# Performance work log

Measured on AMD Instinct MI355X. Metric: run time of the kernel, lower is better.

Reference implementation:

```python
import jax, jax.numpy as jnp
import numpy as np

D_MODEL = 512
NUM_HEADS = 8
D_K = D_MODEL // NUM_HEADS


def setup_inputs() -> dict:
    key = jax.random.key(0)
    kx, kq, kk, kv, ko = jax.random.split(key, 5)
    scale = 1.0 / np.sqrt(D_MODEL)
    return {
        "x": jax.random.normal(kx, (2, 4096, D_MODEL), dtype=jnp.float32),
        "Wq": jax.random.normal(kq, (D_MODEL, D_MODEL), dtype=jnp.float32) * scale,
        "Wk": jax.random.normal(kk, (D_MODEL, D_MODEL), dtype=jnp.float32) * scale,
        "Wv": jax.random.normal(kv, (D_MODEL, D_MODEL), dtype=jnp.float32) * scale,
        "Wo": jax.random.normal(ko, (D_MODEL, D_MODEL), dtype=jnp.float32) * scale,
    }


def reference(x, Wq, Wk, Wv, Wo):
    B, T, D = x.shape
    H, dk = NUM_HEADS, D_K
    # Linear(d,d, bias=False): y = x @ W.T ; weights stored [out,in] like torch
    q = (x @ Wq.T).reshape(B, T, H, dk).transpose(0, 2, 1, 3)  # [B,H,T,dk]
    k = (x @ Wk.T).reshape(B, T, H, dk).transpose(0, 2, 1, 3)
    v = (x @ Wv.T).reshape(B, T, H, dk).transpose(0, 2, 1, 3)
    scores = jnp.einsum("bhqd,bhkd->bhqk", q, k) / np.sqrt(dk)  # [B,H,T,T]
    probs = jax.nn.softmax(scores, axis=-1)
    o = jnp.einsum("bhqk,bhkd->bhqd", probs, v)  # [B,H,T,dk]
    o = o.transpose(0, 2, 1, 3).reshape(B, T, D)
    return o @ Wo.T
```

## Files before the change

### kernel.cpp

```cpp
#include <hip/hip_runtime.h>
#include <hip/hip_bf16.h>

#define SEQ 4096
#define DMODEL 512
#define HEADS 8
#define DK 64
#define BATCH 2
#define MTOT (BATCH * SEQ)
#define NBH (BATCH * HEADS)

typedef __attribute__((ext_vector_type(8))) short bh8;
typedef __attribute__((ext_vector_type(4))) float f4;
typedef __attribute__((ext_vector_type(16))) float f16x;
typedef __attribute__((ext_vector_type(2))) float f2;

#define MFMA(a, b, c)   __builtin_amdgcn_mfma_f32_16x16x32_bf16(a, b, c, 0, 0, 0)
#define MFMA32(a, b, c) __builtin_amdgcn_mfma_f32_32x32x16_bf16(a, b, c, 0, 0, 0)
#define GLL16(g, l) __builtin_amdgcn_global_load_lds( \
    (const __attribute__((address_space(1))) void*)(g), \
    (__attribute__((address_space(3))) void*)(l), 16, 0, 0)

__device__ __forceinline__ unsigned short f2b(float f) {
    union { float f; unsigned u; } v; v.f = f;
    unsigned r = v.u + 0x7fff + ((v.u >> 16) & 1);
    return (unsigned short)(r >> 16);
}

__device__ __forceinline__ unsigned cvtpk(float lo, float hi) {
    unsigned r;
    asm("v_cvt_pk_bf16_f32 %0, %1, %2" : "=v"(r) : "v"(lo), "v"(hi));
    return r;
}
__device__ __forceinline__ void plswap(unsigned& a, unsigned& b) {
    asm("v_permlane32_swap_b32 %0, %1" : "+v"(a), "+v"(b));
}
__device__ __forceinline__ float wave_max_pair(float x) {
    float b = x; asm("" : "+v"(b));
    float a = x;
    asm("v_permlane32_swap_b32 %0, %1" : "+v"(a), "+v"(b));
    return fmaxf(a, b);
}
__device__ __forceinline__ float wave_sum_pair(float x) {
    float b = x; asm("" : "+v"(b));
    float a = x;
    asm("v_permlane32_swap_b32 %0, %1" : "+v"(a), "+v"(b));
    return a + b;
}
__device__ __forceinline__ f2 pk_add(f2 a, f2 b) {
    f2 d; asm("v_pk_add_f32 %0, %1, %2" : "=v"(d) : "v"(a), "v"(b)); return d;
}
__device__ __forceinline__ f2 pk_mul(f2 a, f2 b) {
    f2 d; asm("v_pk_mul_f32 %0, %1, %2" : "=v"(d) : "v"(a), "v"(b)); return d;
}
__device__ __forceinline__ float max3f(float a, float b, float c) {
    float d; asm("v_max3_f32 %0, %1, %2, %3" : "=v"(d) : "v"(a), "v"(b), "v"(c));
    return d;
}

__global__ __launch_bounds__(256) void convert_k(
    const float* __restrict__ x, const float* __restrict__ wq,
    const float* __restrict__ wk, const float* __restrict__ wv,
    const float* __restrict__ wo, unsigned short* __restrict__ dst)
{
    const size_t i = ((size_t)blockIdx.x * 256 + threadIdx.x) * 4;
    const float* s; size_t o;
    if (i < 4194304u)                 { s = x;  o = i; }
    else if (i < 4194304u + 262144u)  { s = wq; o = i - 4194304u; }
    else if (i < 4194304u + 524288u)  { s = wk; o = i - (4194304u + 262144u); }
    else if (i < 4194304u + 786432u)  { s = wv; o = i - (4194304u + 524288u); }
    else                              { s = wo; o = i - (4194304u + 786432u); }
    float4 v = *(const float4*)(s + o);
    ushort4 u; u.x = f2b(v.x); u.y = f2b(v.y); u.z = f2b(v.z); u.w = f2b(v.w);
    *(ushort4*)(dst + i) = u;
}

__global__ __launch_bounds__(256) void qkv_gemm_mfma(
    const unsigned short* __restrict__ xb,
    const unsigned short* __restrict__ Wb,
    unsigned short* __restrict__ QKV)
{
    const int z = blockIdx.z;
    const unsigned short* A = xb;
    const unsigned short* B = Wb + (size_t)z * (DMODEL * DMODEL);
    const int m0 = blockIdx.x * 128, n0 = blockIdx.y * 128;
    const int tid = threadIdx.x, w = tid >> 6, l = tid & 63;
    const int wr = w >> 1, wc = w & 1;

    __shared__ __align__(16) unsigned short As[128 * 32];
    __shared__ __align__(16) unsigned short Bs[128 * 32];

    f4 acc[4][4] = {};
    const int lrow = l >> 2, lslot = l & 3;

    for (int k0 = 0; k0 < DMODEL; k0 += 32) {
        __syncthreads();
        #pragma unroll
        for (int j = 0; j < 2; ++j) {
            const int row = w * 32 + j * 16 + lrow;
            const int sw = lslot ^ ((row >> 1) & 3);
            GLL16(A + (size_t)(m0 + row) * DMODEL + k0 + sw * 8,
                  (char*)As + (w * 32 + j * 16) * 64);
            GLL16(B + (size_t)(n0 + row) * DMODEL + k0 + sw * 8,
                  (char*)Bs + (w * 32 + j * 16) * 64);
        }
        __syncthreads();
        bh8 af[4], bg[4];
        #pragma unroll
        for (int mi = 0; mi < 4; ++mi) {
            const int r = wr * 64 + mi * 16 + (l & 15);
            af[mi] = *(const bh8*)((const char*)As + r * 64 +
                                   (((l >> 4) * 16) ^ (((r >> 1) & 3) << 4)));
        }
        #pragma unroll
        for (int ni = 0; ni < 4; ++ni) {
            const int r = wc * 64 + ni * 16 + (l & 15);
            bg[ni] = *(const bh8*)((const char*)Bs + r * 64 +
                                   (((l >> 4) * 16) ^ (((r >> 1) & 3) << 4)));
        }
        #pragma unroll
        for (int mi = 0; mi < 4; ++mi)
            #pragma unroll
            for (int ni = 0; ni < 4; ++ni)
                acc[mi][ni] = MFMA(af[mi], bg[ni], acc[mi][ni]);
    }

    unsigned short* Out = QKV + (size_t)z * ((size_t)NBH * SEQ * DK);
    const float sc = (z == 0) ? 0.18033688011112042f : 1.0f;
    #pragma unroll
    for (int mi = 0; mi < 4; ++mi) {
        #pragma unroll
        for (int rg = 0; rg < 4; ++rg) {
            const int m = m0 + wr * 64 + mi * 16 + (l >> 4) * 4 + rg;
            const int b = m >> 12, t = m & (SEQ - 1);
            #pragma unroll
            for (int ni = 0; ni < 4; ++ni) {
                const int n = n0 + wc * 64 + ni * 16 + (l & 15);
                const int h = n >> 6, d = n & 63;
                Out[(((size_t)(b * HEADS + h)) * SEQ + t) * DK + d] =
                    f2b(acc[mi][ni][rg] * sc);
            }
        }
    }
}

__global__ __launch_bounds__(256) void vtrans(
    const unsigned short* __restrict__ Vh, unsigned short* __restrict__ Vt)
{
    const int bh = blockIdx.y, t0 = blockIdx.x * 64;
    __shared__ unsigned short L[64][72];
    const unsigned short* src = Vh + ((size_t)bh * SEQ + t0) * DK;
    const int r = threadIdx.x >> 3, c8 = (threadIdx.x & 7) * 8;
    #pragma unroll
    for (int it = 0; it < 2; ++it) {
        const int row = r + it * 32;
        ushort4 a = *(const ushort4*)(src + (size_t)row * DK + c8);
        ushort4 b = *(const ushort4*)(src + (size_t)row * DK + c8 + 4);
        L[row][c8 + 0] = a.x; L[row][c8 + 1] = a.y; L[row][c8 + 2] = a.z; L[row][c8 + 3] = a.w;
        L[row][c8 + 4] = b.x; L[row][c8 + 5] = b.y; L[row][c8 + 6] = b.z; L[row][c8 + 7] = b.w;
    }
    __syncthreads();
    unsigned short* dst = Vt + (size_t)bh * DK * SEQ + t0;
    #pragma unroll
    for (int it = 0; it < 2; ++it) {
        const int d = r + it * 32;
        ushort4 a, b;
        a.x = L[c8 + 0][d]; a.y = L[c8 + 1][d]; a.z = L[c8 + 2][d]; a.w = L[c8 + 3][d];
        b.x = L[c8 + 4][d]; b.y = L[c8 + 5][d]; b.z = L[c8 + 6][d]; b.w = L[c8 + 7][d];
        *(ushort4*)(dst + (size_t)d * SEQ + c8) = a;
        *(ushort4*)(dst + (size_t)d * SEQ + c8 + 4) = b;
    }
}

__global__ __launch_bounds__(256) void flash_mfma(
    const unsigned short* __restrict__ Qh,
    const unsigned short* __restrict__ Kh,
    const unsigned short* __restrict__ Vtp,
    unsigned short* __restrict__ Ow)
{
    const int bid = blockIdx.x;
    const int bh = bid & 15, q0 = (bid >> 4) * 128;
    const int tid = threadIdx.x, w = tid >> 6, l = tid & 63;
    const int lq = l & 31, hi = l >> 5;

    __shared__ __align__(16) char lds[32768];

    const unsigned short* Qb = Qh + (size_t)bh * SEQ * DK;
    const unsigned short* Kb = Kh + (size_t)bh * SEQ * DK;
    const unsigned short* Vb = Vtp + (size_t)bh * DK * SEQ;

    bh8 qf[4];
    #pragma unroll
    for (int ks = 0; ks < 4; ++ks)
        qf[ks] = *(const bh8*)(Qb + (size_t)(q0 + w * 32 + lq) * DK + ks * 16 + hi * 8);

    int koff[2], voff[2];
    #pragma unroll
    for (int j = 0; j < 2; ++j) {
        const int f = 2 * w + j, rh = f >> 2, ks = f & 3;
        koff[j] = (rh * 32 + lq) * DK + ks * 16 + hi * 8;
        voff[j] = (rh * 32 + lq) * SEQ + ks * 16 + hi * 8;
    }

    f16x o0 = {}, o1 = {};
    float m_run = -3.0e38f, l_run = 0.f;

#define STAGE(buf, kv0_) do {                                             \
    _Pragma("unroll")                                                     \
    for (int j_ = 0; j_ < 2; ++j_) {                                      \
        GLL16(Kb + (size_t)(kv0_) * DK + koff[j_],                        \
              lds + (buf) * 16384 + (2 * w + j_) * 1024);                 \
        GLL16(Vb + (size_t)(kv0_) + voff[j_],                             \
              lds + (buf) * 16384 + 8192 + (2 * w + j_) * 1024);          \
    }                                                                     \
} while (0)

    STAGE(0, 0);
    __syncthreads();
    int cur = 0;
    const char* myfrag = lds + l * 16;

    for (int t = 0; t < SEQ / 64; ++t) {
        if (t < SEQ / 64 - 1) STAGE(cur ^ 1, (t + 1) * 64);

        const char* kb = myfrag + cur * 16384;

        f16x sa0 = {}, sa1 = {};
        __builtin_amdgcn_s_setprio(1);
        #pragma unroll
        for (int ks = 0; ks < 4; ++ks) {
            bh8 k0 = *(const bh8*)(kb + ks * 1024);
            bh8 k1 = *(const bh8*)(kb + (4 + ks) * 1024);
            sa0 = MFMA32(k0, qf[ks], sa0);
            sa1 = MFMA32(k1, qf[ks], sa1);
        }
        __builtin_amdgcn_s_setprio(0);

        float a = fmaxf(sa0[0], sa0[1]);
        float b = fmaxf(sa1[0], sa1[1]);
        #pragma unroll
        for (int r = 2; r < 16; r += 2) {
            a = max3f(a, sa0[r], sa0[r + 1]);
            b = max3f(b, sa1[r], sa1[r + 1]);
        }
        const float mx = wave_max_pair(fmaxf(a, b));

        const bool skip = __all(mx <= m_run + 8.0f);
        float mnew = m_run, corr = 1.0f;
        if (!skip) {
            mnew = fmaxf(m_run, mx);
            corr = __builtin_amdgcn_exp2f(m_run - mnew);
        }

        union uf { f16x v; f2 h[8]; };
        uf U0, U1; U0.v = sa0; U1.v = sa1;
        f2 nm2; nm2[0] = -mnew; nm2[1] = -mnew;
        f2 p2[16];
        #pragma unroll
        for (int i = 0; i < 8; ++i) {
            f2 t0 = pk_add(U0.h[i], nm2);
            f2 t1 = pk_add(U1.h[i], nm2);
            f2 e0, e1;
            e0[0] = __builtin_amdgcn_exp2f(t0[0]);
            e0[1] = __builtin_amdgcn_exp2f(t0[1]);
            e1[0] = __builtin_amdgcn_exp2f(t1[0]);
            e1[1] = __builtin_amdgcn_exp2f(t1[1]);
            p2[i] = e0; p2[8 + i] = e1;
        }

        f2 s0 = pk_add(p2[0], p2[1]),   s1 = pk_add(p2[2], p2[3]);
        f2 s2 = pk_add(p2[4], p2[5]),   s3 = pk_add(p2[6], p2[7]);
        f2 s4 = pk_add(p2[8], p2[9]),   s5 = pk_add(p2[10], p2[11]);
        f2 s6 = pk_add(p2[12], p2[13]), s7 = pk_add(p2[14], p2[15]);
        s0 = pk_add(s0, s1); s2 = pk_add(s2, s3);
        s4 = pk_add(s4, s5); s6 = pk_add(s6, s7);
        s0 = pk_add(s0, s2); s4 = pk_add(s4, s6);
        s0 = pk_add(s0, s4);
        const float psum = wave_sum_pair(s0[0] + s0[1]);

        if (!skip) {
            m_run = mnew;
            l_run = l_run * corr + psum;
            f2 c2; c2[0] = corr; c2[1] = corr;
            uf O0, O1; O0.v = o0; O1.v = o1;
            #pragma unroll
            for (int i = 0; i < 8; ++i) {
                O0.h[i] = pk_mul(O0.h[i], c2);
                O1.h[i] = pk_mul(O1.h[i], c2);
            }
            o0 = O0.v; o1 = O1.v;
        } else {
            l_run += psum;
        }

        bh8 pf[4];
        #pragma unroll
        for (int cb = 0; cb < 2; ++cb) {
            unsigned k0 = cvtpk(p2[8 * cb + 0][0], p2[8 * cb + 0][1]);
            unsigned k1 = cvtpk(p2[8 * cb + 1][0], p2[8 * cb + 1][1]);
            unsigned k2 = cvtpk(p2[8 * cb + 2][0], p2[8 * cb + 2][1]);
            unsigned k3 = cvtpk(p2[8 * cb + 3][0], p2[8 * cb + 3][1]);
            unsigned k4 = cvtpk(p2[8 * cb + 4][0], p2[8 * cb + 4][1]);
            unsigned k5 = cvtpk(p2[8 * cb + 5][0], p2[8 * cb + 5][1]);
            unsigned k6 = cvtpk(p2[8 * cb + 6][0], p2[8 * cb + 6][1]);
            unsigned k7 = cvtpk(p2[8 * cb + 7][0], p2[8 * cb + 7][1]);
            plswap(k0, k2); plswap(k1, k3); plswap(k4, k6); plswap(k5, k7);
            union { unsigned u[4]; bh8 v; } f0, f1;
            f0.u[0] = k0; f0.u[1] = k1; f0.u[2] = k2; f0.u[3] = k3;
            f1.u[0] = k4; f1.u[1] = k5; f1.u[2] = k6; f1.u[3] = k7;
            pf[cb * 2 + 0] = f0.v;
            pf[cb * 2 + 1] = f1.v;
        }

        const char* vb = myfrag + cur * 16384 + 8192;
        __builtin_amdgcn_s_setprio(1);
        #pragma unroll
        for (int ks = 0; ks < 4; ++ks) {
            bh8 v0 = *(const bh8*)(vb + ks * 1024);
            bh8 v1 = *(const bh8*)(vb + (4 + ks) * 1024);
            o0 = MFMA32(v0, pf[ks], o0);
            o1 = MFMA32(v1, pf[ks], o1);
        }
        __builtin_amdgcn_s_setprio(0);

        __syncthreads();
        cur ^= 1;
    }
#undef STAGE

    const float inv = 1.0f / l_run;
    char* Tb = lds + w * 4096;
    #pragma unroll
    for (int db = 0; db < 2; ++db) {
        f16x ov = db ? o1 : o0;
        #pragma unroll
        for (int j = 0; j < 8; ++j) {
            const int r = 2 * j;
            const int d = db * 32 + (r & 3) + 8 * (r >> 2) + 4 * hi;
            unsigned pk = cvtpk(ov[r] * inv, ov[r + 1] * inv);
            *(unsigned*)(Tb + lq * 128 + ((d * 2) ^ ((lq & 7) << 4))) = pk;
        }
    }
    __syncthreads();
    const int b = bh >> 3, h = bh & 7;
    const int row = l >> 1, half = l & 1;
    const int q = q0 + w * 32 + row;
    unsigned short* dst = Ow + ((size_t)b * SEQ + q) * DMODEL + h * DK + half * 32;
    #pragma unroll
    for (int i = 0; i < 4; ++i) {
        const int byte = (half * 64 + i * 16) ^ ((row & 7) << 4);
        uint4 vv = *(const uint4*)(Tb + row * 128 + byte);
        *(uint4*)(dst + i * 8) = vv;
    }
}

__global__ __launch_bounds__(256) void out_gemm_mfma(
    const unsigned short* __restrict__ Ob,
    const unsigned short* __restrict__ Wob,
    float* __restrict__ out)
{
    const int m0 = blockIdx.x * 128, n0 = blockIdx.y * 128;
    const int tid = threadIdx.x, w = tid >> 6, l = tid & 63;
    const int wr = w >> 1, wc = w & 1;

    __shared__ __align__(16) unsigned short As[128 * 32];
    __shared__ __align__(16) unsigned short Bs[128 * 32];

    f4 acc[4][4] = {};
    const int lrow = l >> 2, lslot = l & 3;

    for (int k0 = 0; k0 < DMODEL; k0 += 32) {
        __syncthreads();
        #pragma unroll
        for (int j = 0; j < 2; ++j) {
            const int row = w * 32 + j * 16 + lrow;
            const int sw = lslot ^ ((row >> 1) & 3);
            GLL16(Ob + (size_t)(m0 + row) * DMODEL + k0 + sw * 8,
                  (char*)As + (w * 32 + j * 16) * 64);
            GLL16(Wob + (size_t)(n0 + row) * DMODEL + k0 + sw * 8,
                  (char*)Bs + (w * 32 + j * 16) * 64);
        }
        __syncthreads();
        bh8 af[4], bg[4];
        #pragma unroll
        for (int mi = 0; mi < 4; ++mi) {
            const int r = wr * 64 + mi * 16 + (l & 15);
            af[mi] = *(const bh8*)((const char*)As + r * 64 +
                                   (((l >> 4) * 16) ^ (((r >> 1) & 3) << 4)));
        }
        #pragma unroll
        for (int ni = 0; ni < 4; ++ni) {
            const int r = wc * 64 + ni * 16 + (l & 15);
            bg[ni] = *(const bh8*)((const char*)Bs + r * 64 +
                                   (((l >> 4) * 16) ^ (((r >> 1) & 3) << 4)));
        }
        #pragma unroll
        for (int mi = 0; mi < 4; ++mi)
            #pragma unroll
            for (int ni = 0; ni < 4; ++ni)
                acc[mi][ni] = MFMA(af[mi], bg[ni], acc[mi][ni]);
    }

    #pragma unroll
    for (int mi = 0; mi < 4; ++mi) {
        #pragma unroll
        for (int rg = 0; rg < 4; ++rg) {
            const int m = m0 + wr * 64 + mi * 16 + (l >> 4) * 4 + rg;
            #pragma unroll
            for (int ni = 0; ni < 4; ++ni) {
                const int n = n0 + wc * 64 + ni * 16 + (l & 15);
                out[(size_t)m * DMODEL + n] = acc[mi][ni][rg];
            }
        }
    }
}

extern "C" void kernel_launch(void* const* d_in, const int* in_sizes, int n_in,
                              void* d_out, int out_size, void* d_ws, size_t ws_size,
                              hipStream_t stream)
{
    const float* x  = (const float*)d_in[0];
    const float* Wq = (const float*)d_in[1];
    const float* Wk = (const float*)d_in[2];
    const float* Wv = (const float*)d_in[3];
    const float* Wo = (const float*)d_in[4];
    float* out = (float*)d_out;

    unsigned short* ws = (unsigned short*)d_ws;
    unsigned short* xb  = ws;
    unsigned short* Wb  = xb + 4194304;
    unsigned short* QKV = Wb + 4 * 262144;
    unsigned short* Vt  = QKV + 3 * 4194304;
    unsigned short* Ow  = Vt + 4194304;
    unsigned short* Qh = QKV;
    unsigned short* Kh = QKV + 4194304;
    unsigned short* Vh = QKV + 2 * 4194304;

    convert_k<<<5120, 256, 0, stream>>>(x, Wq, Wk, Wv, Wo, ws);
    qkv_gemm_mfma<<<dim3(MTOT / 128, DMODEL / 128, 3), 256, 0, stream>>>(xb, Wb, QKV);
    vtrans<<<dim3(SEQ / 64, NBH), 256, 0, stream>>>(Vh, Vt);
    flash_mfma<<<512, 256, 0, stream>>>(Qh, Kh, Vt, Ow);
    out_gemm_mfma<<<dim3(MTOT / 128, DMODEL / 128), 256, 0, stream>>>(
        Ow, Wb + 3 * 262144, out);
}
```

Baseline: 154.0 us.

## Split KV sequence into two interleaved streams with independent softmax states

Each wave now runs two independent online-softmax streams over the two halves of the key/value sequence, interleaving their QK^T and softmax/PV phases within every iteration, and merges them at the end with rescaling. This exposes more instruction-level parallelism so MFMA work of one stream can overlap with the exp/reduction work of the other, and halves the number of loop iterations and barriers. The cost is doubled LDS usage (64 KB) and more accumulator registers, which can lower occupancy. A launch-bounds hint of two blocks per CU is added.

```diff
diff --git a/kernel.cpp b/kernel.cpp
--- a/kernel.cpp
+++ b/kernel.cpp
@@ -13,6 +13,8 @@
 typedef __attribute__((ext_vector_type(4))) float f4;
 typedef __attribute__((ext_vector_type(16))) float f16x;
 typedef __attribute__((ext_vector_type(2))) float f2;
+
+union uf { f16x v; f2 h[8]; };
 
 #define MFMA(a, b, c)   __builtin_amdgcn_mfma_f32_16x16x32_bf16(a, b, c, 0, 0, 0)
 #define MFMA32(a, b, c) __builtin_amdgcn_mfma_f32_32x32x16_bf16(a, b, c, 0, 0, 0)
@@ -171,7 +173,7 @@
     }
 }
 
-__global__ __launch_bounds__(256) void flash_mfma(
+__global__ __launch_bounds__(256, 2) void flash_mfma(
     const unsigned short* __restrict__ Qh,
     const unsigned short* __restrict__ Kh,
     const unsigned short* __restrict__ Vtp,
@@ -182,7 +184,7 @@
     const int tid = threadIdx.x, w = tid >> 6, l = tid & 63;
     const int lq = l & 31, hi = l >> 5;
 
-    __shared__ __align__(16) char lds[32768];
+    __shared__ __align__(16) char lds[65536];
 
     const unsigned short* Qb = Qh + (size_t)bh * SEQ * DK;
     const unsigned short* Kb = Kh + (size_t)bh * SEQ * DK;
@@ -201,133 +203,151 @@
         voff[j] = (rh * 32 + lq) * SEQ + ks * 16 + hi * 8;
     }
 
-    f16x o0 = {}, o1 = {};
-    float m_run = -3.0e38f, l_run = 0.f;
-
-#define STAGE(buf, kv0_) do {                                             \
-    _Pragma("unroll")                                                     \
-    for (int j_ = 0; j_ < 2; ++j_) {                                      \
-        GLL16(Kb + (size_t)(kv0_) * DK + koff[j_],                        \
-              lds + (buf) * 16384 + (2 * w + j_) * 1024);                 \
-        GLL16(Vb + (size_t)(kv0_) + voff[j_],                             \
-              lds + (buf) * 16384 + 8192 + (2 * w + j_) * 1024);          \
-    }                                                                     \
+    f16x oA0 = {}, oA1 = {}, oB0 = {}, oB1 = {};
+    float mA = -3.0e38f, lA = 0.f, mB = -3.0e38f, lB = 0.f;
+
+#define STAGE(buf_, half_, kv0_) do {                                         \
+    _Pragma("unroll")                                                         \
+    for (int j_ = 0; j_ < 2; ++j_) {                                          \
+        GLL16(Kb + (size_t)(half_) * (2048 * DK) + (size_t)(kv0_) * DK + koff[j_], \
+              lds + (buf_) * 32768 + (half_) * 16384 + (2 * w + j_) * 1024);  \
+        GLL16(Vb + (half_) * 2048 + (size_t)(kv0_) + voff[j_],                \
+              lds + (buf_) * 32768 + (half_) * 16384 + 8192 + (2 * w + j_) * 1024); \
+    }                                                                         \
 } while (0)
 
-    STAGE(0, 0);
+#define QKT(kb_, sa0_, sa1_) do {                                             \
+    __builtin_amdgcn_s_setprio(1);                                            \
+    _Pragma("unroll")                                                         \
+    for (int ks_ = 0; ks_ < 4; ++ks_) {                                       \
+        bh8 k0_ = *(const bh8*)((kb_) + ks_ * 1024);                          \
+        bh8 k1_ = *(const bh8*)((kb_) + (4 + ks_) * 1024);                    \
+        sa0_ = MFMA32(k0_, qf[ks_], sa0_);                                    \
+        sa1_ = MFMA32(k1_, qf[ks_], sa1_);                                    \
+    }                                                                         \
+    __builtin_amdgcn_s_setprio(0);                                            \
+} while (0)
+
+#define SMPV(vb_, sa0_, sa1_, m_run_, l_run_, o0_, o1_) do {                  \
+    float a_ = fmaxf(sa0_[0], sa0_[1]);                                       \
+    float b_ = fmaxf(sa1_[0], sa1_[1]);                                       \
+    _Pragma("unroll")                                                         \
+    for (int r_ = 2; r_ < 16; r_ += 2) {                                      \
+        a_ = max3f(a_, sa0_[r_], sa0_[r_ + 1]);                               \
+        b_ = max3f(b_, sa1_[r_], sa1_[r_ + 1]);                               \
+    }                                                                         \
+    const float mx_ = wave_max_pair(fmaxf(a_, b_));                           \
+    const bool skip_ = __all(mx_ <= m_run_ + 8.0f);                           \
+    float mnew_ = m_run_, corr_ = 1.0f;                                       \
+    if (!skip_) {                                                             \
+        mnew_ = fmaxf(m_run_, mx_);                                           \
+        corr_ = __builtin_amdgcn_exp2f(m_run_ - mnew_);                       \
+    }                                                                         \
+    uf U0_, U1_; U0_.v = sa0_; U1_.v = sa1_;                                  \
+    f2 nm2_; nm2_[0] = -mnew_; nm2_[1] = -mnew_;                              \
+    f2 p2_[16];                                                               \
+    _Pragma("unroll")                                                         \
+    for (int i_ = 0; i_ < 8; ++i_) {                                          \
+        f2 t0_ = pk_add(U0_.h[i_], nm2_);                                     \
+        f2 t1_ = pk_add(U1_.h[i_], nm2_);                                     \
+        f2 e0_, e1_;                                                          \
+        e0_[0] = __builtin_amdgcn_exp2f(t0_[0]);                              \
+        e0_[1] = __builtin_amdgcn_exp2f(t0_[1]);                              \
+        e1_[0] = __builtin_amdgcn_exp2f(t1_[0]);                              \
+        e1_[1] = __builtin_amdgcn_exp2f(t1_[1]);                              \
+        p2_[i_] = e0_; p2_[8 + i_] = e1_;                                     \
+    }                                                                         \
+    f2 s0_ = pk_add(p2_[0], p2_[1]),   s1_ = pk_add(p2_[2], p2_[3]);          \
+    f2 s2_ = pk_add(p2_[4], p2_[5]),   s3_ = pk_add(p2_[6], p2_[7]);          \
+    f2 s4_ = pk_add(p2_[8], p2_[9]),   s5_ = pk_add(p2_[10], p2_[11]);        \
+    f2 s6_ = pk_add(p2_[12], p2_[13]), s7_ = pk_add(p2_[14], p2_[15]);        \
+    s0_ = pk_add(s0_, s1_); s2_ = pk_add(s2_, s3_);                           \
+    s4_ = pk_add(s4_, s5_); s6_ = pk_add(s6_, s7_);                           \
+    s0_ = pk_add(s0_, s2_); s4_ = pk_add(s4_, s6_);                           \
+    s0_ = pk_add(s0_, s4_);                                                   \
+    const float psum_ = wave_sum_pair(s0_[0] + s0_[1]);                       \
+    if (!skip_) {                                                             \
+        m_run_ = mnew_;                                                       \
+        l_run_ = l_run_ * corr_ + psum_;                                      \
+        f2 c2_; c2_[0] = corr_; c2_[1] = corr_;                               \
+        uf O0_, O1_; O0_.v = o0_; O1_.v = o1_;                                \
+        _Pragma("unroll")                                                     \
+        for (int i_ = 0; i_ < 8; ++i_) {                                      \
+            O0_.h[i_] = pk_mul(O0_.h[i_], c2_);                               \
+            O1_.h[i_] = pk_mul(O1_.h[i_], c2_);                               \
+        }                                                                     \
+        o0_ = O0_.v; o1_ = O1_.v;                                             \
+    } else {                                                                  \
+        l_run_ += psum_;                                                      \
+    }                                                                         \
+    bh8 pf_[4];                                                               \
+    _Pragma("unroll")                                                         \
+    for (int cb_ = 0; cb_ < 2; ++cb_) {                                       \
+        unsigned k0_ = cvtpk(p2_[8 * cb_ + 0][0], p2_[8 * cb_ + 0][1]);       \
+        unsigned k1_ = cvtpk(p2_[8 * cb_ + 1][0], p2_[8 * cb_ + 1][1]);       \
+        unsigned k2_ = cvtpk(p2_[8 * cb_ + 2][0], p2_[8 * cb_ + 2][1]);       \
+        unsigned k3_ = cvtpk(p2_[8 * cb_ + 3][0], p2_[8 * cb_ + 3][1]);       \
+        unsigned k4_ = cvtpk(p2_[8 * cb_ + 4][0], p2_[8 * cb_ + 4][1]);       \
+        unsigned k5_ = cvtpk(p2_[8 * cb_ + 5][0], p2_[8 * cb_ + 5][1]);       \
+        unsigned k6_ = cvtpk(p2_[8 * cb_ + 6][0], p2_[8 * cb_ + 6][1]);       \
+        unsigned k7_ = cvtpk(p2_[8 * cb_ + 7][0], p2_[8 * cb_ + 7][1]);       \
+        plswap(k0_, k2_); plswap(k1_, k3_); plswap(k4_, k6_); plswap(k5_, k7_);\
+        union { unsigned u[4]; bh8 v; } f0_, f1_;                             \
+        f0_.u[0] = k0_; f0_.u[1] = k1_; f0_.u[2] = k2_; f0_.u[3] = k3_;       \
+        f1_.u[0] = k4_; f1_.u[1] = k5_; f1_.u[2] = k6_; f1_.u[3] = k7_;       \
+        pf_[cb_ * 2 + 0] = f0_.v;                                             \
+        pf_[cb_ * 2 + 1] = f1_.v;                                             \
+    }                                                                         \
+    __builtin_amdgcn_s_setprio(1);                                            \
+    _Pragma("unroll")                                                         \
+    for (int ks_ = 0; ks_ < 4; ++ks_) {                                       \
+        bh8 v0_ = *(const bh8*)((vb_) + ks_ * 1024);                          \
+        bh8 v1_ = *(const bh8*)((vb_) + (4 + ks_) * 1024);                    \
+        o0_ = MFMA32(v0_, pf_[ks_], o0_);                                     \
+        o1_ = MFMA32(v1_, pf_[ks_], o1_);                                     \
+    }                                                                         \
+    __builtin_amdgcn_s_setprio(0);                                            \
+} while (0)
+
+    STAGE(0, 0, 0);
+    STAGE(0, 1, 0);
     __syncthreads();
     int cur = 0;
     const char* myfrag = lds + l * 16;
 
-    for (int t = 0; t < SEQ / 64; ++t) {
-        if (t < SEQ / 64 - 1) STAGE(cur ^ 1, (t + 1) * 64);
-
-        const char* kb = myfrag + cur * 16384;
-
-        f16x sa0 = {}, sa1 = {};
-        __builtin_amdgcn_s_setprio(1);
-        #pragma unroll
-        for (int ks = 0; ks < 4; ++ks) {
-            bh8 k0 = *(const bh8*)(kb + ks * 1024);
-            bh8 k1 = *(const bh8*)(kb + (4 + ks) * 1024);
-            sa0 = MFMA32(k0, qf[ks], sa0);
-            sa1 = MFMA32(k1, qf[ks], sa1);
-        }
-        __builtin_amdgcn_s_setprio(0);
-
-        float a = fmaxf(sa0[0], sa0[1]);
-        float b = fmaxf(sa1[0], sa1[1]);
-        #pragma unroll
-        for (int r = 2; r < 16; r += 2) {
-            a = max3f(a, sa0[r], sa0[r + 1]);
-            b = max3f(b, sa1[r], sa1[r + 1]);
-        }
-        const float mx = wave_max_pair(fmaxf(a, b));
-
-        const bool skip = __all(mx <= m_run + 8.0f);
-        float mnew = m_run, corr = 1.0f;
-        if (!skip) {
-            mnew = fmaxf(m_run, mx);
-            corr = __builtin_amdgcn_exp2f(m_run - mnew);
-        }
-
-        union uf { f16x v; f2 h[8]; };
-        uf U0, U1; U0.v = sa0; U1.v = sa1;
-        f2 nm2; nm2[0] = -mnew; nm2[1] = -mnew;
-        f2 p2[16];
-        #pragma unroll
-        for (int i = 0; i < 8; ++i) {
-            f2 t0 = pk_add(U0.h[i], nm2);
-            f2 t1 = pk_add(U1.h[i], nm2);
-            f2 e0, e1;
-            e0[0] = __builtin_amdgcn_exp2f(t0[0]);
-            e0[1] = __builtin_amdgcn_exp2f(t0[1]);
-            e1[0] = __builtin_amdgcn_exp2f(t1[0]);
-            e1[1] = __builtin_amdgcn_exp2f(t1[1]);
-            p2[i] = e0; p2[8 + i] = e1;
-        }
-
-        f2 s0 = pk_add(p2[0], p2[1]),   s1 = pk_add(p2[2], p2[3]);
-        f2 s2 = pk_add(p2[4], p2[5]),   s3 = pk_add(p2[6], p2[7]);
-        f2 s4 = pk_add(p2[8], p2[9]),   s5 = pk_add(p2[10], p2[11]);
-        f2 s6 = pk_add(p2[12], p2[13]), s7 = pk_add(p2[14], p2[15]);
-        s0 = pk_add(s0, s1); s2 = pk_add(s2, s3);
-        s4 = pk_add(s4, s5); s6 = pk_add(s6, s7);
-        s0 = pk_add(s0, s2); s4 = pk_add(s4, s6);
-        s0 = pk_add(s0, s4);
-        const float psum = wave_sum_pair(s0[0] + s0[1]);
-
-        if (!skip) {
-            m_run = mnew;
-            l_run = l_run * corr + psum;
-            f2 c2; c2[0] = corr; c2[1] = corr;
-            uf O0, O1; O0.v = o0; O1.v = o1;
-            #pragma unroll
-            for (int i = 0; i < 8; ++i) {
-                O0.h[i] = pk_mul(O0.h[i], c2);
-                O1.h[i] = pk_mul(O1.h[i], c2);
-            }
-            o0 = O0.v; o1 = O1.v;
-        } else {
-            l_run += psum;
-        }
-
-        bh8 pf[4];
-        #pragma unroll
-        for (int cb = 0; cb < 2; ++cb) {
-            unsigned k0 = cvtpk(p2[8 * cb + 0][0], p2[8 * cb + 0][1]);
-            unsigned k1 = cvtpk(p2[8 * cb + 1][0], p2[8 * cb + 1][1]);
-            unsigned k2 = cvtpk(p2[8 * cb + 2][0], p2[8 * cb + 2][1]);
-            unsigned k3 = cvtpk(p2[8 * cb + 3][0], p2[8 * cb + 3][1]);
-            unsigned k4 = cvtpk(p2[8 * cb + 4][0], p2[8 * cb + 4][1]);
-            unsigned k5 = cvtpk(p2[8 * cb + 5][0], p2[8 * cb + 5][1]);
-            unsigned k6 = cvtpk(p2[8 * cb + 6][0], p2[8 * cb + 6][1]);
-            unsigned k7 = cvtpk(p2[8 * cb + 7][0], p2[8 * cb + 7][1]);
-            plswap(k0, k2); plswap(k1, k3); plswap(k4, k6); plswap(k5, k7);
-            union { unsigned u[4]; bh8 v; } f0, f1;
-            f0.u[0] = k0; f0.u[1] = k1; f0.u[2] = k2; f0.u[3] = k3;
-            f1.u[0] = k4; f1.u[1] = k5; f1.u[2] = k6; f1.u[3] = k7;
-            pf[cb * 2 + 0] = f0.v;
-            pf[cb * 2 + 1] = f1.v;
-        }
-
-        const char* vb = myfrag + cur * 16384 + 8192;
-        __builtin_amdgcn_s_setprio(1);
-        #pragma unroll
-        for (int ks = 0; ks < 4; ++ks) {
-            bh8 v0 = *(const bh8*)(vb + ks * 1024);
-            bh8 v1 = *(const bh8*)(vb + (4 + ks) * 1024);
-            o0 = MFMA32(v0, pf[ks], o0);
-            o1 = MFMA32(v1, pf[ks], o1);
-        }
-        __builtin_amdgcn_s_setprio(0);
+    for (int t = 0; t < 32; ++t) {
+        if (t < 31) {
+            STAGE(cur ^ 1, 0, (t + 1) * 64);
+            STAGE(cur ^ 1, 1, (t + 1) * 64);
+        }
+
+        const char* kbA = myfrag + cur * 32768;
+        const char* kbB = kbA + 16384;
+
+        f16x sA0 = {}, sA1 = {}, sB0 = {}, sB1 = {};
+        QKT(kbA, sA0, sA1);
+        QKT(kbB, sB0, sB1);
+        SMPV(kbA + 8192, sA0, sA1, mA, lA, oA0, oA1);
+        SMPV(kbB + 8192, sB0, sB1, mB, lB, oB0, oB1);
 
         __syncthreads();
         cur ^= 1;
     }
 #undef STAGE
-
-    const float inv = 1.0f / l_run;
+#undef QKT
+#undef SMPV
+
+    const float mt = fmaxf(mA, mB);
+    const float cA = __builtin_amdgcn_exp2f(mA - mt);
+    const float cB = __builtin_amdgcn_exp2f(mB - mt);
+    f16x o0, o1;
+    #pragma unroll
+    for (int r = 0; r < 16; ++r) {
+        o0[r] = oA0[r] * cA + oB0[r] * cB;
+        o1[r] = oA1[r] * cA + oB1[r] * cB;
+    }
+    const float inv = 1.0f / (lA * cA + lB * cB);
+
     char* Tb = lds + w * 4096;
     #pragma unroll
     for (int db = 0; db < 2; ++db) {
```

Measured after the change: 141.0 us. 1.09x faster.

## Split attention KV range into two partitions, load K/V directly, add merge kernel

Applied to the files above, without the earlier changes.

The flash kernel now splits each query tile's KV sequence into two halves, doubling the grid to 1024 blocks. Each block writes an unnormalised bf16 partial output plus per-row max and sum, and a new merge kernel combines the two partials and normalises them. Each wave also loads its K and V fragments straight from global memory into registers instead of staging them through double-buffered LDS, which removes the per-iteration barrier. The cost is extra global traffic for the partials, redundant K/V loads across the four waves of a block, and load latency that is no longer hidden by explicit prefetching.

```diff
diff --git a/kernel.cpp b/kernel.cpp
--- a/kernel.cpp
+++ b/kernel.cpp
@@ -14,6 +14,8 @@
 typedef __attribute__((ext_vector_type(16))) float f16x;
 typedef __attribute__((ext_vector_type(2))) float f2;
 
+union uf { f16x v; f2 h[8]; };
+
 #define MFMA(a, b, c)   __builtin_amdgcn_mfma_f32_16x16x32_bf16(a, b, c, 0, 0, 0)
 #define MFMA32(a, b, c) __builtin_amdgcn_mfma_f32_32x32x16_bf16(a, b, c, 0, 0, 0)
 #define GLL16(g, l) __builtin_amdgcn_global_load_lds( \
@@ -24,6 +26,12 @@
     union { float f; unsigned u; } v; v.f = f;
     unsigned r = v.u + 0x7fff + ((v.u >> 16) & 1);
     return (unsigned short)(r >> 16);
+}
+__device__ __forceinline__ float lo2f(unsigned u) {
+    union { unsigned u; float f; } v; v.u = u << 16; return v.f;
+}
+__device__ __forceinline__ float hi2f(unsigned u) {
+    union { unsigned u; float f; } v; v.u = u & 0xffff0000u; return v.f;
 }
 
 __device__ __forceinline__ unsigned cvtpk(float lo, float hi) {
@@ -171,18 +179,22 @@
     }
 }
 
-__global__ __launch_bounds__(256) void flash_mfma(
+__global__ __launch_bounds__(256) void flash_direct(
     const unsigned short* __restrict__ Qh,
     const unsigned short* __restrict__ Kh,
     const unsigned short* __restrict__ Vtp,
-    unsigned short* __restrict__ Ow)
+    unsigned short* __restrict__ P0,
+    unsigned short* __restrict__ P1,
+    float* __restrict__ MLp)
 {
     const int bid = blockIdx.x;
-    const int bh = bid & 15, q0 = (bid >> 4) * 128;
+    const int bh = bid & 15, qt = (bid >> 4) & 31, kvp = bid >> 9;
+    const int q0 = qt * 128;
     const int tid = threadIdx.x, w = tid >> 6, l = tid & 63;
     const int lq = l & 31, hi = l >> 5;
-
-    __shared__ __align__(16) char lds[32768];
+    const int kvbase = kvp * 2048;
+
+    __shared__ __align__(16) char lds[16384];
 
     const unsigned short* Qb = Qh + (size_t)bh * SEQ * DK;
     const unsigned short* Kb = Kh + (size_t)bh * SEQ * DK;
@@ -193,65 +205,54 @@
     for (int ks = 0; ks < 4; ++ks)
         qf[ks] = *(const bh8*)(Qb + (size_t)(q0 + w * 32 + lq) * DK + ks * 16 + hi * 8);
 
-    int koff[2], voff[2];
-    #pragma unroll
-    for (int j = 0; j < 2; ++j) {
-        const int f = 2 * w + j, rh = f >> 2, ks = f & 3;
-        koff[j] = (rh * 32 + lq) * DK + ks * 16 + hi * 8;
-        voff[j] = (rh * 32 + lq) * SEQ + ks * 16 + hi * 8;
-    }
+    const unsigned short* Kl0 = Kb + (size_t)(kvbase + lq) * DK + hi * 8;
+    const unsigned short* Kl1 = Kb + (size_t)(kvbase + 32 + lq) * DK + hi * 8;
+    const unsigned short* Vl0 = Vb + (size_t)lq * SEQ + kvbase + hi * 8;
+    const unsigned short* Vl1 = Vb + (size_t)(32 + lq) * SEQ + kvbase + hi * 8;
 
     f16x o0 = {}, o1 = {};
     float m_run = -3.0e38f, l_run = 0.f;
 
-#define STAGE(buf, kv0_) do {                                             \
-    _Pragma("unroll")                                                     \
-    for (int j_ = 0; j_ < 2; ++j_) {                                      \
-        GLL16(Kb + (size_t)(kv0_) * DK + koff[j_],                        \
-              lds + (buf) * 16384 + (2 * w + j_) * 1024);                 \
-        GLL16(Vb + (size_t)(kv0_) + voff[j_],                             \
-              lds + (buf) * 16384 + 8192 + (2 * w + j_) * 1024);          \
-    }                                                                     \
-} while (0)
-
-    STAGE(0, 0);
-    __syncthreads();
-    int cur = 0;
-    const char* myfrag = lds + l * 16;
-
-    for (int t = 0; t < SEQ / 64; ++t) {
-        if (t < SEQ / 64 - 1) STAGE(cur ^ 1, (t + 1) * 64);
-
-        const char* kb = myfrag + cur * 16384;
+    for (int t = 0; t < 32; ++t) {
+        const int kv0 = t * 64;
+
+        bh8 kf0[4], kf1[4];
+        #pragma unroll
+        for (int ks = 0; ks < 4; ++ks) {
+            kf0[ks] = *(const bh8*)(Kl0 + (size_t)kv0 * DK + ks * 16);
+            kf1[ks] = *(const bh8*)(Kl1 + (size_t)kv0 * DK + ks * 16);
+        }
 
         f16x sa0 = {}, sa1 = {};
         __builtin_amdgcn_s_setprio(1);
         #pragma unroll
         for (int ks = 0; ks < 4; ++ks) {
-            bh8 k0 = *(const bh8*)(kb + ks * 1024);
-            bh8 k1 = *(const bh8*)(kb + (4 + ks) * 1024);
-            sa0 = MFMA32(k0, qf[ks], sa0);
-            sa1 = MFMA32(k1, qf[ks], sa1);
+            sa0 = MFMA32(kf0[ks], qf[ks], sa0);
+            sa1 = MFMA32(kf1[ks], qf[ks], sa1);
         }
         __builtin_amdgcn_s_setprio(0);
 
-        float a = fmaxf(sa0[0], sa0[1]);
-        float b = fmaxf(sa1[0], sa1[1]);
+        bh8 vf0[4], vf1[4];
+        #pragma unroll
+        for (int ks = 0; ks < 4; ++ks) {
+            vf0[ks] = *(const bh8*)(Vl0 + kv0 + ks * 16);
+            vf1[ks] = *(const bh8*)(Vl1 + kv0 + ks * 16);
+        }
+
+        float a_ = fmaxf(sa0[0], sa0[1]);
+        float b_ = fmaxf(sa1[0], sa1[1]);
         #pragma unroll
         for (int r = 2; r < 16; r += 2) {
-            a = max3f(a, sa0[r], sa0[r + 1]);
-            b = max3f(b, sa1[r], sa1[r + 1]);
-        }
-        const float mx = wave_max_pair(fmaxf(a, b));
-
+            a_ = max3f(a_, sa0[r], sa0[r + 1]);
+            b_ = max3f(b_, sa1[r], sa1[r + 1]);
+        }
+        const float mx = wave_max_pair(fmaxf(a_, b_));
         const bool skip = __all(mx <= m_run + 8.0f);
         float mnew = m_run, corr = 1.0f;
         if (!skip) {
             mnew = fmaxf(m_run, mx);
             corr = __builtin_amdgcn_exp2f(m_run - mnew);
         }
-
-        union uf { f16x v; f2 h[8]; };
         uf U0, U1; U0.v = sa0; U1.v = sa1;
         f2 nm2; nm2[0] = -mnew; nm2[1] = -mnew;
         f2 p2[16];
@@ -266,7 +267,6 @@
             e1[1] = __builtin_amdgcn_exp2f(t1[1]);
             p2[i] = e0; p2[8 + i] = e1;
         }
-
         f2 s0 = pk_add(p2[0], p2[1]),   s1 = pk_add(p2[2], p2[3]);
         f2 s2 = pk_add(p2[4], p2[5]),   s3 = pk_add(p2[6], p2[7]);
         f2 s4 = pk_add(p2[8], p2[9]),   s5 = pk_add(p2[10], p2[11]);
@@ -276,7 +276,6 @@
         s0 = pk_add(s0, s2); s4 = pk_add(s4, s6);
         s0 = pk_add(s0, s4);
         const float psum = wave_sum_pair(s0[0] + s0[1]);
-
         if (!skip) {
             m_run = mnew;
             l_run = l_run * corr + psum;
@@ -311,23 +310,15 @@
             pf[cb * 2 + 1] = f1.v;
         }
 
-        const char* vb = myfrag + cur * 16384 + 8192;
         __builtin_amdgcn_s_setprio(1);
         #pragma unroll
         for (int ks = 0; ks < 4; ++ks) {
-            bh8 v0 = *(const bh8*)(vb + ks * 1024);
-            bh8 v1 = *(const bh8*)(vb + (4 + ks) * 1024);
-            o0 = MFMA32(v0, pf[ks], o0);
-            o1 = MFMA32(v1, pf[ks], o1);
+            o0 = MFMA32(vf0[ks], pf[ks], o0);
+            o1 = MFMA32(vf1[ks], pf[ks], o1);
         }
         __builtin_amdgcn_s_setprio(0);
-
-        __syncthreads();
-        cur ^= 1;
-    }
-#undef STAGE
-
-    const float inv = 1.0f / l_run;
+    }
+
     char* Tb = lds + w * 4096;
     #pragma unroll
     for (int db = 0; db < 2; ++db) {
@@ -336,20 +327,69 @@
         for (int j = 0; j < 8; ++j) {
             const int r = 2 * j;
             const int d = db * 32 + (r & 3) + 8 * (r >> 2) + 4 * hi;
-            unsigned pk = cvtpk(ov[r] * inv, ov[r + 1] * inv);
+            unsigned pk = cvtpk(ov[r], ov[r + 1]);
             *(unsigned*)(Tb + lq * 128 + ((d * 2) ^ ((lq & 7) << 4))) = pk;
         }
     }
     __syncthreads();
-    const int b = bh >> 3, h = bh & 7;
+    unsigned short* po = kvp ? P1 : P0;
     const int row = l >> 1, half = l & 1;
-    const int q = q0 + w * 32 + row;
-    unsigned short* dst = Ow + ((size_t)b * SEQ + q) * DMODEL + h * DK + half * 32;
+    const int qloc = w * 32 + row;
+    unsigned short* dst = po + (((size_t)bh * 32 + qt) * 128 + qloc) * 64 + half * 32;
     #pragma unroll
     for (int i = 0; i < 4; ++i) {
         const int byte = (half * 64 + i * 16) ^ ((row & 7) << 4);
-        uint4 vv = *(const uint4*)(Tb + row * 128 + byte);
-        *(uint4*)(dst + i * 8) = vv;
+        *(uint4*)(dst + i * 8) = *(const uint4*)(Tb + row * 128 + byte);
+    }
+    if (hi == 0) {
+        float* mlb = MLp + (((size_t)kvp * 16 + bh) * 32 + qt) * 256;
+        mlb[w * 32 + lq] = m_run;
+        mlb[128 + w * 32 + lq] = l_run;
+    }
+}
+
+__global__ __launch_bounds__(256) void merge_k(
+    const unsigned short* __restrict__ P0,
+    const unsigned short* __restrict__ P1,
+    const float* __restrict__ MLp,
+    unsigned short* __restrict__ Ow)
+{
+    const int qt = blockIdx.x, bh = blockIdx.y;
+    const int tid = threadIdx.x;
+    __shared__ float C0[128], C1[128];
+    if (tid < 128) {
+        const float* m0b = MLp + (((size_t)bh) * 32 + qt) * 256;
+        const float* m1b = MLp + (((size_t)16 + bh) * 32 + qt) * 256;
+        const float m0 = m0b[tid], l0 = m0b[128 + tid];
+        const float m1 = m1b[tid], l1 = m1b[128 + tid];
+        const float m = fmaxf(m0, m1);
+        const float c0 = __builtin_amdgcn_exp2f(m0 - m);
+        const float c1 = __builtin_amdgcn_exp2f(m1 - m);
+        const float inv = 1.0f / (l0 * c0 + l1 * c1);
+        C0[tid] = c0 * inv;
+        C1[tid] = c1 * inv;
+    }
+    __syncthreads();
+    const int q = tid >> 1, half = tid & 1;
+    const float c0 = C0[q], c1 = C1[q];
+    const size_t off = (((size_t)bh * 32 + qt) * 128 + q) * 64 + half * 32;
+    const int b = bh >> 3, h = bh & 7;
+    unsigned short* dst = Ow + ((size_t)b * SEQ + qt * 128 + q) * DMODEL + h * DK + half * 32;
+    #pragma unroll
+    for (int i = 0; i < 4; ++i) {
+        uint4 a = *(const uint4*)(P0 + off + i * 8);
+        uint4 bb = *(const uint4*)(P1 + off + i * 8);
+        uint4 o;
+        unsigned* ap = (unsigned*)&a;
+        unsigned* bp = (unsigned*)&bb;
+        unsigned* op = (unsigned*)&o;
+        #pragma unroll
+        for (int k = 0; k < 4; ++k) {
+            const unsigned ua = ap[k], ub = bp[k];
+            op[k] = cvtpk(lo2f(ua) * c0 + lo2f(ub) * c1,
+                          hi2f(ua) * c0 + hi2f(ub) * c1);
+        }
+        *(uint4*)(dst + i * 8) = o;
     }
 }
 
@@ -435,10 +475,15 @@
     unsigned short* Kh = QKV + 4194304;
     unsigned short* Vh = QKV + 2 * 4194304;
 
+    unsigned short* P0 = xb;
+    unsigned short* P1 = Vh;
+    float* MLp = (float*)Wb;
+
     convert_k<<<5120, 256, 0, stream>>>(x, Wq, Wk, Wv, Wo, ws);
     qkv_gemm_mfma<<<dim3(MTOT / 128, DMODEL / 128, 3), 256, 0, stream>>>(xb, Wb, QKV);
     vtrans<<<dim3(SEQ / 64, NBH), 256, 0, stream>>>(Vh, Vt);
-    flash_mfma<<<512, 256, 0, stream>>>(Qh, Kh, Vt, Ow);
+    flash_direct<<<1024, 256, 0, stream>>>(Qh, Kh, Vt, P0, P1, MLp);
+    merge_k<<<dim3(32, 16), 256, 0, stream>>>(P0, P1, MLp, Ow);
     out_gemm_mfma<<<dim3(MTOT / 128, DMODEL / 128), 256, 0, stream>>>(
         Ow, Wb + 3 * 262144, out);
 }
```

Result: slower. 286.9 us (+86.3%).
